# Kernel tuning notes

Hardware: AMD Instinct MI355X
Metric: run time of the kernel (lower is better)

## Reference

```python
import jax, jax.numpy as jnp
import numpy as np

B, S, D, H, L = 2, 2048, 1024, 16, 4
HD = D // H
EPS = 1e-6
ROPE_BASE = 10000.0


def rms_norm(x, w):
    v = jnp.mean(x.astype(jnp.float32) ** 2, axis=-1, keepdims=True)
    return (w * (x.astype(jnp.float32) * jax.lax.rsqrt(v + EPS))).astype(x.dtype)


def rotate_half(x):
    x1, x2 = jnp.split(x, 2, axis=-1)
    return jnp.concatenate([-x2, x1], axis=-1)


def setup_inputs() -> dict:
    key = jax.random.key(0)
    ks = jax.random.split(key, 8)
    x = jax.random.normal(ks[0], (B, S, D), jnp.float32)
    time_deltas = jax.random.uniform(ks[1], (B, S), jnp.float32)
    # causal multiplicative mask [B, S, S]
    attn_mask = jnp.broadcast_to(jnp.tril(jnp.ones((S, S), jnp.float32)), (B, S, S))
    sd = 0.02
    uvqk_w = jax.random.normal(ks[2], (L, D, 4 * D), jnp.float32) * sd
    uvqk_b = jnp.zeros((L, 4 * D), jnp.float32)
    gate_w = jnp.ones((L, D), jnp.float32)
    out_w = jax.random.normal(ks[3], (L, D, D), jnp.float32) * sd
    out_b = jnp.zeros((L, D), jnp.float32)
    in_norm_w = jnp.ones((D,), jnp.float32)
    last_norm_w = jnp.ones((D,), jnp.float32)
    position_ids = jnp.broadcast_to(jnp.arange(S, dtype=jnp.int32), (B, S))
    return {"x": x, "time_deltas": time_deltas, "attn_mask": attn_mask,
            "uvqk_w": uvqk_w, "uvqk_b": uvqk_b, "gate_w": gate_w,
            "out_w": out_w, "out_b": out_b, "in_norm_w": in_norm_w,
            "last_norm_w": last_norm_w, "position_ids": position_ids}


def reference(x, time_deltas, attn_mask, uvqk_w, uvqk_b, gate_w, out_w, out_b,
              in_norm_w, last_norm_w, position_ids):
    # RotaryEmbedding: combined position = pos + 0.1*log(dt+1)
    inv_freq = 1.0 / ROPE_BASE ** (jnp.arange(0, HD, 2, dtype=jnp.float32) / HD)
    pos = position_ids.astype(jnp.float32) + jnp.log(time_deltas + 1.0) * 0.1
    freqs = pos[..., None] * inv_freq                      # [B,S,HD/2]
    emb = jnp.concatenate([freqs, freqs], axis=-1)          # [B,S,HD]
    cos = jnp.cos(emb)[:, :, None, :]                       # [B,S,1,HD]
    sin = jnp.sin(emb)[:, :, None, :]

    scale = 1.0 / np.sqrt(HD).astype(np.float32)
    h = rms_norm(x, in_norm_w)
    for l in range(L):
        residual = h
        uvqk = h @ uvqk_w[l] + uvqk_b[l]                    # [B,S,4D]
        u, v, q, k = jnp.split(uvqk, 4, axis=-1)
        u = jax.nn.silu(u)
        q = q.reshape(B, S, H, HD)
        k = k.reshape(B, S, H, HD)
        v = v.reshape(B, S, H, HD)
        q = q * cos + rotate_half(q) * sin
        k = k * cos + rotate_half(k) * sin
        scores = jnp.einsum('bqhd,bkhd->bhqk', q, k) * scale
        w = jax.nn.silu(scores) * attn_mask[:, None, :, :]  # SiLU attn, masked
        attn = jnp.einsum('bhqk,bkhd->bqhd', w, v).reshape(B, S, D)
        gated = rms_norm(attn, gate_w[l]) * u
        h = residual + gated @ out_w[l] + out_b[l]
    return rms_norm(h, last_norm_w)
```

## Files before the change

kernel.cpp:

```cpp
#include <hip/hip_runtime.h>
#include <hip/hip_bf16.h>
#include <math.h>

#define BB 2
#define SS 2048
#define DD 1024
#define HH 16
#define HD 64
#define LL 4
#define BS (BB * SS)
#define FOURD (4 * DD)

typedef unsigned int u32;
typedef unsigned short ushort_t;
typedef __attribute__((ext_vector_type(8))) short bf16x8;
typedef __attribute__((ext_vector_type(4))) float f32x4;

__device__ __forceinline__ float silu_f(float x) {
    return x / (1.0f + expf(-x));
}
__device__ __forceinline__ float silu_fast(float x) {
    return x / (1.0f + __expf(-x));
}

__device__ __forceinline__ ushort_t f2bf(float x) {
    u32 u = __float_as_uint(x);
    u32 r = (u + 0x7fffu + ((u >> 16) & 1u)) >> 16;
    return (ushort_t)r;
}
__device__ __forceinline__ float bf2f(ushort_t h) {
    return __uint_as_float((u32)h << 16);
}

typedef __attribute__((address_space(3))) u32 lds_u32;
typedef const __attribute__((address_space(1))) u32 glb_u32;
__device__ __forceinline__ void gload16(const void* g, const void* lds) {
    __builtin_amdgcn_global_load_lds((glb_u32*)(uintptr_t)g,
                                     (lds_u32*)(uintptr_t)lds, 16, 0, 0);
}

#define MFMA16(a, b, c) __builtin_amdgcn_mfma_f32_16x16x32_bf16((a), (b), (c), 0, 0, 0)

union U8 { u32 d[4]; bf16x8 v; };

__global__ __launch_bounds__(256) void rope_table_kernel(
    const float* __restrict__ td, const int* __restrict__ pid,
    float* __restrict__ cosT, float* __restrict__ sinT)
{
    int idx = blockIdx.x * blockDim.x + threadIdx.x;
    if (idx >= BS * 32) return;
    int i = idx & 31, bs = idx >> 5;
    float pos = (float)pid[bs] + 0.1f * logf(td[bs] + 1.0f);
    float inv = powf(10000.0f, -(float)(2 * i) / 64.0f);
    float f = pos * inv;
    float c = cosf(f), s = sinf(f);
    cosT[bs * HD + i] = c;  cosT[bs * HD + i + 32] = c;
    sinT[bs * HD + i] = s;  sinT[bs * HD + i + 32] = s;
}

__global__ __launch_bounds__(256) void rmsnorm_kernel(
    const float* __restrict__ in, const float* __restrict__ w,
    const float* __restrict__ mul, int mulStride,
    float* __restrict__ out,
    ushort_t* __restrict__ hi, ushort_t* __restrict__ lo)
{
    __shared__ float red[4];
    int row = blockIdx.x, t = threadIdx.x;
    const float4 v = *(const float4*)&in[(size_t)row * DD + t * 4];
    float ss = v.x * v.x + v.y * v.y + v.z * v.z + v.w * v.w;
    #pragma unroll
    for (int o = 32; o > 0; o >>= 1) ss += __shfl_down(ss, o);
    if ((t & 63) == 0) red[t >> 6] = ss;
    __syncthreads();
    float tot = red[0] + red[1] + red[2] + red[3];
    float r = rsqrtf(tot * (1.0f / (float)DD) + 1e-6f);
    const float4 wv = *(const float4*)&w[t * 4];
    float4 o4;
    o4.x = v.x * r * wv.x;  o4.y = v.y * r * wv.y;
    o4.z = v.z * r * wv.z;  o4.w = v.w * r * wv.w;
    if (mul) {
        const float4 m = *(const float4*)&mul[(size_t)row * mulStride + t * 4];
        o4.x *= m.x; o4.y *= m.y; o4.z *= m.z; o4.w *= m.w;
    }
    const size_t o = (size_t)row * DD + t * 4;
    *(float4*)&out[o] = o4;
    if (hi) {
        ushort4 h4, l4;
        float e;
        h4.x = f2bf(o4.x); e = o4.x - bf2f(h4.x); l4.x = f2bf(e);
        h4.y = f2bf(o4.y); e = o4.y - bf2f(h4.y); l4.y = f2bf(e);
        h4.z = f2bf(o4.z); e = o4.z - bf2f(h4.z); l4.z = f2bf(e);
        h4.w = f2bf(o4.w); e = o4.w - bf2f(h4.w); l4.w = f2bf(e);
        *(ushort4*)&hi[o] = h4;
        *(ushort4*)&lo[o] = l4;
    }
}

__global__ __launch_bounds__(256) void wsplit_kernel(
    const float* __restrict__ W, ushort_t* __restrict__ hi,
    ushort_t* __restrict__ lo, int K, int N)
{
    __shared__ float T[32][33];
    const int n0 = blockIdx.x * 32, k0 = blockIdx.y * 32;
    const int t = threadIdx.x;
    {
        const int r = t >> 3, cg = (t & 7) * 4;
        const float4 v = *(const float4*)&W[(size_t)(k0 + r) * N + n0 + cg];
        T[r][cg] = v.x; T[r][cg + 1] = v.y; T[r][cg + 2] = v.z; T[r][cg + 3] = v.w;
    }
    __syncthreads();
    {
        const int n = t >> 3, kg = (t & 7) * 4;
        ushort4 h4, l4;
        float x, e;
        x = T[kg + 0][n]; h4.x = f2bf(x); e = x - bf2f(h4.x); l4.x = f2bf(e);
        x = T[kg + 1][n]; h4.y = f2bf(x); e = x - bf2f(h4.y); l4.y = f2bf(e);
        x = T[kg + 2][n]; h4.z = f2bf(x); e = x - bf2f(h4.z); l4.z = f2bf(e);
        x = T[kg + 3][n]; h4.w = f2bf(x); e = x - bf2f(h4.w); l4.w = f2bf(e);
        const size_t o = (size_t)(n0 + n) * K + k0 + kg;
        *(ushort4*)&hi[o] = h4;
        *(ushort4*)&lo[o] = l4;
    }
}

#define TBM 128
#define TBN 128
#define TBK 32
__global__ __launch_bounds__(256) void gemm3_kernel(
    const ushort_t* __restrict__ Ah, const ushort_t* __restrict__ Al,
    const ushort_t* __restrict__ Bh, const ushort_t* __restrict__ Bl,
    const float* __restrict__ bias, const float* __restrict__ res,
    float* __restrict__ C, ushort_t* __restrict__ Chi, ushort_t* __restrict__ Clo,
    int M, int N, int K)
{
    __shared__ ushort_t sAh[TBM][TBK];
    __shared__ ushort_t sAl[TBM][TBK];
    __shared__ ushort_t sBh[TBN][TBK];
    __shared__ ushort_t sBl[TBN][TBK];

    const int tid = threadIdx.x;
    const int w = tid >> 6, l = tid & 63;
    const int wr = w >> 1, wc = w & 1;
    const int m0 = blockIdx.y * TBM, n0 = blockIdx.x * TBN;
    const int lr = l & 15, lk = (l >> 4) * 8;

    f32x4 acc[4][4];
    #pragma unroll
    for (int m = 0; m < 4; ++m)
        #pragma unroll
        for (int n = 0; n < 4; ++n)
            acc[m][n] = (f32x4){0.f, 0.f, 0.f, 0.f};

    for (int k0 = 0; k0 < K; k0 += TBK) {
        if (k0) __syncthreads();
        #pragma unroll
        for (int i = 0; i < 2; ++i) {
            const int cb = i * 256 + w * 64;
            const int chunk = cb + l;
            const int row = chunk >> 2;
            const int kc = (chunk & 3) * 8;
            const size_t ga = (size_t)(m0 + row) * K + k0 + kc;
            const size_t gb = (size_t)(n0 + row) * K + k0 + kc;
            gload16(Ah + ga, &sAh[0][0] + (size_t)cb * 8);
            gload16(Al + ga, &sAl[0][0] + (size_t)cb * 8);
            gload16(Bh + gb, &sBh[0][0] + (size_t)cb * 8);
            gload16(Bl + gb, &sBl[0][0] + (size_t)cb * 8);
        }
        __syncthreads();

        bf16x8 ah[4], al[4], bh[4], bl[4];
        #pragma unroll
        for (int m = 0; m < 4; ++m) {
            ah[m] = *(const bf16x8*)&sAh[wr * 64 + m * 16 + lr][lk];
            al[m] = *(const bf16x8*)&sAl[wr * 64 + m * 16 + lr][lk];
        }
        #pragma unroll
        for (int n = 0; n < 4; ++n) {
            bh[n] = *(const bf16x8*)&sBh[wc * 64 + n * 16 + lr][lk];
            bl[n] = *(const bf16x8*)&sBl[wc * 64 + n * 16 + lr][lk];
        }
        #pragma unroll
        for (int m = 0; m < 4; ++m) {
            #pragma unroll
            for (int n = 0; n < 4; ++n) {
                acc[m][n] = MFMA16(ah[m], bh[n], acc[m][n]);
                acc[m][n] = MFMA16(al[m], bh[n], acc[m][n]);
                acc[m][n] = MFMA16(ah[m], bl[n], acc[m][n]);
            }
        }
    }

    #pragma unroll
    for (int m = 0; m < 4; ++m) {
        #pragma unroll
        for (int n = 0; n < 4; ++n) {
            const int col = n0 + wc * 64 + n * 16 + lr;
            #pragma unroll
            for (int r = 0; r < 4; ++r) {
                const int row = m0 + wr * 64 + m * 16 + (l >> 4) * 4 + r;
                const size_t o = (size_t)row * N + col;
                float v = acc[m][n][r] + bias[col];
                if (res) v += res[o];
                C[o] = v;
                if (Chi) {
                    ushort_t hv = f2bf(v);
                    Chi[o] = hv;
                    Clo[o] = f2bf(v - bf2f(hv));
                }
            }
        }
    }
}

__global__ __launch_bounds__(256) void postproc_kernel(
    float* __restrict__ uvqk,
    const float* __restrict__ cosT, const float* __restrict__ sinT,
    ushort_t* __restrict__ q_hi, ushort_t* __restrict__ q_lo,
    ushort_t* __restrict__ k_hi, ushort_t* __restrict__ k_lo)
{
    const int bs = blockIdx.x, t = threadIdx.x;
    const int b = bs >> 11, s = bs & (SS - 1);
    float* base = uvqk + (size_t)bs * FOURD;

    float4 u = *(float4*)&base[t * 4];
    u.x = silu_f(u.x); u.y = silu_f(u.y); u.z = silu_f(u.z); u.w = silu_f(u.w);
    *(float4*)&base[t * 4] = u;

    const int hh = t >> 4, p = (t & 15) * 2;
    const float c0 = cosT[bs * HD + p], c1 = cosT[bs * HD + p + 1];
    const float s0 = sinT[bs * HD + p], s1 = sinT[bs * HD + p + 1];
    const size_t hrow = ((size_t)(b * HH + hh) * SS + s) * HD;
    #pragma unroll
    for (int sect = 2; sect <= 3; ++sect) {
        const float* qp = base + sect * DD + hh * HD;
        const float a0 = qp[p], a1 = qp[p + 1];
        const float b0 = qp[p + 32], b1 = qp[p + 33];
        float o0 = a0 * c0 - b0 * s0;
        float o1 = a1 * c1 - b1 * s1;
        float o2 = b0 * c0 + a0 * s0;
        float o3 = b1 * c1 + a1 * s1;
        ushort_t* dh = (sect == 2) ? q_hi : k_hi;
        ushort_t* dl = (sect == 2) ? q_lo : k_lo;
        ushort_t hv;
        hv = f2bf(o0); dh[hrow + p]      = hv; dl[hrow + p]      = f2bf(o0 - bf2f(hv));
        hv = f2bf(o1); dh[hrow + p + 1]  = hv; dl[hrow + p + 1]  = f2bf(o1 - bf2f(hv));
        hv = f2bf(o2); dh[hrow + p + 32] = hv; dl[hrow + p + 32] = f2bf(o2 - bf2f(hv));
        hv = f2bf(o3); dh[hrow + p + 33] = hv; dl[hrow + p + 33] = f2bf(o3 - bf2f(hv));
    }
}

__global__ __launch_bounds__(256) void vtrans_kernel(
    const float* __restrict__ uvqk,
    ushort_t* __restrict__ vT_hi, ushort_t* __restrict__ vT_lo)
{
    __shared__ float T[64][65];
    const int sb = blockIdx.x, h = blockIdx.y, b = blockIdx.z;
    const int t = threadIdx.x;
    const int s0 = sb * 64;
    #pragma unroll
    for (int it = 0; it < 4; ++it) {
        const int idx = it * 256 + t;
        const int row = idx >> 4, c4 = (idx & 15) * 4;
        const float4 v = *(const float4*)&uvqk[
            (size_t)(b * SS + s0 + row) * FOURD + DD + h * HD + c4];
        T[row][c4] = v.x; T[row][c4 + 1] = v.y;
        T[row][c4 + 2] = v.z; T[row][c4 + 3] = v.w;
    }
    __syncthreads();
    const int d = t >> 2, sc = (t & 3) * 16;
    u32 hw[8], lw[8];
    #pragma unroll
    for (int j = 0; j < 8; ++j) {
        const float x0 = T[sc + 2 * j][d];
        const float x1 = T[sc + 2 * j + 1][d];
        const ushort_t h0 = f2bf(x0), h1 = f2bf(x1);
        hw[j] = (u32)h0 | ((u32)h1 << 16);
        lw[j] = (u32)f2bf(x0 - bf2f(h0)) | ((u32)f2bf(x1 - bf2f(h1)) << 16);
    }
    const size_t o = ((size_t)(b * HH + h) * HD + d) * SS + s0 + sc;
    *(uint4*)&vT_hi[o] = make_uint4(hw[0], hw[1], hw[2], hw[3]);
    *(uint4*)&vT_hi[o + 8] = make_uint4(hw[4], hw[5], hw[6], hw[7]);
    *(uint4*)&vT_lo[o] = make_uint4(lw[0], lw[1], lw[2], lw[3]);
    *(uint4*)&vT_lo[o + 8] = make_uint4(lw[4], lw[5], lw[6], lw[7]);
}

__global__ __launch_bounds__(256) void attn_kernel(
    const ushort_t* __restrict__ q_hi, const ushort_t* __restrict__ q_lo,
    const ushort_t* __restrict__ k_hi, const ushort_t* __restrict__ k_lo,
    const ushort_t* __restrict__ vT_hi, const ushort_t* __restrict__ vT_lo,
    float* __restrict__ attnOut)
{
    __shared__ ushort_t sKh[2][64 * 64];
    __shared__ ushort_t sKl[2][64 * 64];
    __shared__ ushort_t sVh[2][64 * 64];
    __shared__ ushort_t sVl[2][64 * 64];

    const int qt = (SS / 128 - 1) - blockIdx.x;
    const int h = blockIdx.y, b = blockIdx.z;
    const int tid = threadIdx.x;
    const int w = tid >> 6, l = tid & 63;
    const int lr = l & 15, g = l >> 4;

    const size_t headQ = ((size_t)(b * HH + h) * SS) * HD;
    const size_t headV = ((size_t)(b * HH + h) * HD) * SS;

    bf16x8 qh[2][2], ql[2][2];
    {
        const int qrow0 = qt * 128 + w * 32;
        #pragma unroll
        for (int qf = 0; qf < 2; ++qf)
            #pragma unroll
            for (int ds_ = 0; ds_ < 2; ++ds_) {
                const size_t off = headQ + (size_t)(qrow0 + qf * 16 + lr) * HD
                                   + ds_ * 32 + g * 8;
                qh[qf][ds_] = *(const bf16x8*)&q_hi[off];
                ql[qf][ds_] = *(const bf16x8*)&q_lo[off];
            }
    }

    f32x4 acc[2][4];
    #pragma unroll
    for (int qf = 0; qf < 2; ++qf)
        #pragma unroll
        for (int df = 0; df < 4; ++df)
            acc[qf][df] = (f32x4){0.f, 0.f, 0.f, 0.f};

    const int nkt = 2 * qt + 2;

#define STAGE_TILE(pb, kt_)                                                    \
    {                                                                          \
        const ushort_t* kbh = k_hi + headQ + (size_t)(kt_) * 64 * HD;          \
        const ushort_t* kbl = k_lo + headQ + (size_t)(kt_) * 64 * HD;          \
        const ushort_t* vbh = vT_hi + headV + (kt_) * 64;                      \
        const ushort_t* vbl = vT_lo + headV + (kt_) * 64;                      \
        _Pragma("unroll")                                                      \
        for (int rep = 0; rep < 2; ++rep) {                                    \
            const int cb = rep * 256 + w * 64;                                 \
            const int chunk = cb + l;                                          \
            const int row = chunk >> 3, dblk = chunk & 7;                      \
            const int sblk = dblk ^ (row & 7);                                 \
            gload16(kbh + (size_t)row * HD + sblk * 8, &sKh[pb][0] + (size_t)cb * 8); \
            gload16(kbl + (size_t)row * HD + sblk * 8, &sKl[pb][0] + (size_t)cb * 8); \
            gload16(vbh + (size_t)row * SS + sblk * 8, &sVh[pb][0] + (size_t)cb * 8); \
            gload16(vbl + (size_t)row * SS + sblk * 8, &sVl[pb][0] + (size_t)cb * 8); \
        }                                                                      \
    }

    STAGE_TILE(0, 0)
    __syncthreads();

    for (int kt = 0; kt < nkt; ++kt) {
        const int pb = kt & 1;
        if (kt + 1 < nkt) STAGE_TILE(pb ^ 1, kt + 1)

        f32x4 sc[4][2];
        #pragma unroll
        for (int f = 0; f < 4; ++f)
            #pragma unroll
            for (int qf = 0; qf < 2; ++qf)
                sc[f][qf] = (f32x4){0.f, 0.f, 0.f, 0.f};

        #pragma unroll
        for (int ds_ = 0; ds_ < 2; ++ds_) {
            bf16x8 kh[4], kl[4];
            #pragma unroll
            for (int f = 0; f < 4; ++f) {
                const int addr = (16 * f + lr) * 64 + (((4 * ds_ + g) ^ (lr & 7)) * 8);
                kh[f] = *(const bf16x8*)&sKh[pb][addr];
                kl[f] = *(const bf16x8*)&sKl[pb][addr];
            }
            #pragma unroll
            for (int f = 0; f < 4; ++f)
                #pragma unroll
                for (int qf = 0; qf < 2; ++qf) {
                    sc[f][qf] = MFMA16(kh[f], qh[qf][ds_], sc[f][qf]);
                    sc[f][qf] = MFMA16(kl[f], qh[qf][ds_], sc[f][qf]);
                    sc[f][qf] = MFMA16(kh[f], ql[qf][ds_], sc[f][qf]);
                }
        }

        u32 pkh[4][2][2], pkl[4][2][2];
        #pragma unroll
        for (int f = 0; f < 4; ++f) {
            #pragma unroll
            for (int qf = 0; qf < 2; ++qf) {
                const int qrow = qt * 128 + w * 32 + qf * 16 + lr;
                float pv[4];
                #pragma unroll
                for (int r = 0; r < 4; ++r) {
                    const int key = kt * 64 + 16 * f + 4 * g + r;
                    const float x = sc[f][qf][r] * 0.125f;
                    pv[r] = (key <= qrow) ? silu_fast(x) : 0.0f;
                }
                #pragma unroll
                for (int t2 = 0; t2 < 2; ++t2) {
                    const ushort_t h0 = f2bf(pv[2 * t2]);
                    const ushort_t h1 = f2bf(pv[2 * t2 + 1]);
                    pkh[f][qf][t2] = (u32)h0 | ((u32)h1 << 16);
                    const float l0 = pv[2 * t2] - bf2f(h0);
                    const float l1 = pv[2 * t2 + 1] - bf2f(h1);
                    pkl[f][qf][t2] = (u32)f2bf(l0) | ((u32)f2bf(l1) << 16);
                }
            }
        }

        #pragma unroll
        for (int s2 = 0; s2 < 2; ++s2) {
            U8 ah[2], al[2];
            #pragma unroll
            for (int qf = 0; qf < 2; ++qf) {
                #pragma unroll
                for (int d = 0; d < 4; ++d) {
                    const int srcLane = lr + 16 * (2 * (g & 1) + (d >> 1));
                    const int t2 = d & 1;
                    int x0 = __shfl((int)pkh[2 * s2][qf][t2], srcLane, 64);
                    int x1 = __shfl((int)pkh[2 * s2 + 1][qf][t2], srcLane, 64);
                    ah[qf].d[d] = (g & 2) ? x1 : x0;
                    x0 = __shfl((int)pkl[2 * s2][qf][t2], srcLane, 64);
                    x1 = __shfl((int)pkl[2 * s2 + 1][qf][t2], srcLane, 64);
                    al[qf].d[d] = (g & 2) ? x1 : x0;
                }
            }
            #pragma unroll
            for (int df = 0; df < 4; ++df) {
                const int vaddr = (16 * df + lr) * 64 + (((4 * s2 + g) ^ (lr & 7)) * 8);
                const bf16x8 vh = *(const bf16x8*)&sVh[pb][vaddr];
                const bf16x8 vl = *(const bf16x8*)&sVl[pb][vaddr];
                #pragma unroll
                for (int qf = 0; qf < 2; ++qf) {
                    acc[qf][df] = MFMA16(ah[qf].v, vh, acc[qf][df]);
                    acc[qf][df] = MFMA16(al[qf].v, vh, acc[qf][df]);
                    acc[qf][df] = MFMA16(ah[qf].v, vl, acc[qf][df]);
                }
            }
        }

        __syncthreads();
    }

    #pragma unroll
    for (int qf = 0; qf < 2; ++qf) {
        #pragma unroll
        for (int df = 0; df < 4; ++df) {
            #pragma unroll
            for (int r = 0; r < 4; ++r) {
                const int row = qt * 128 + w * 32 + qf * 16 + 4 * g + r;
                attnOut[(size_t)(b * SS + row) * DD + h * HD + 16 * df + lr]
                    = acc[qf][df][r];
            }
        }
    }
#undef STAGE_TILE
}

extern "C" void kernel_launch(void* const* d_in, const int* in_sizes, int n_in,
                              void* d_out, int out_size, void* d_ws, size_t ws_size,
                              hipStream_t stream) {
    const float* x           = (const float*)d_in[0];
    const float* td          = (const float*)d_in[1];
    const float* uvqk_w      = (const float*)d_in[3];
    const float* uvqk_b      = (const float*)d_in[4];
    const float* gate_w      = (const float*)d_in[5];
    const float* out_w       = (const float*)d_in[6];
    const float* out_b       = (const float*)d_in[7];
    const float* in_norm_w   = (const float*)d_in[8];
    const float* last_norm_w = (const float*)d_in[9];
    const int*   pid         = (const int*)d_in[10];
    float* out = (float*)d_out;
    char*  ws  = (char*)d_ws;

    const size_t QKV = (size_t)BB * HH * SS * HD;

    float* cosT = (float*)ws;                          ws += (size_t)BS * HD * 4;
    float* sinT = (float*)ws;                          ws += (size_t)BS * HD * 4;
    float* h    = (float*)ws;                          ws += (size_t)BS * DD * 4;
    float* uvqk = (float*)ws;                          ws += (size_t)BS * FOURD * 4;
    float* attn = (float*)ws;                          ws += (size_t)BS * DD * 4;
    ushort_t* h_hi  = (ushort_t*)ws;                   ws += (size_t)BS * DD * 2;
    ushort_t* h_lo  = (ushort_t*)ws;                   ws += (size_t)BS * DD * 2;
    ushort_t* g_hi  = (ushort_t*)ws;                   ws += (size_t)BS * DD * 2;
    ushort_t* g_lo  = (ushort_t*)ws;                   ws += (size_t)BS * DD * 2;
    ushort_t* uWt_hi = (ushort_t*)ws;                  ws += (size_t)FOURD * DD * 2;
    ushort_t* uWt_lo = (ushort_t*)ws;                  ws += (size_t)FOURD * DD * 2;
    ushort_t* oWt_hi = (ushort_t*)ws;                  ws += (size_t)DD * DD * 2;
    ushort_t* oWt_lo = (ushort_t*)ws;                  ws += (size_t)DD * DD * 2;
    ushort_t* q_hi  = (ushort_t*)ws;                   ws += QKV * 2;
    ushort_t* q_lo  = (ushort_t*)ws;                   ws += QKV * 2;
    ushort_t* k_hi  = (ushort_t*)ws;                   ws += QKV * 2;
    ushort_t* k_lo  = (ushort_t*)ws;                   ws += QKV * 2;
    ushort_t* vT_hi = (ushort_t*)ws;                   ws += QKV * 2;
    ushort_t* vT_lo = (ushort_t*)ws;                   ws += QKV * 2;
    (void)ws_size;

    rope_table_kernel<<<(BS * 32 + 255) / 256, 256, 0, stream>>>(td, pid, cosT, sinT);
    rmsnorm_kernel<<<BS, 256, 0, stream>>>(x, in_norm_w, nullptr, 0, h, h_hi, h_lo);

    for (int l = 0; l < LL; ++l) {
        wsplit_kernel<<<dim3(FOURD / 32, DD / 32), 256, 0, stream>>>(
            uvqk_w + (size_t)l * DD * FOURD, uWt_hi, uWt_lo, DD, FOURD);
        gemm3_kernel<<<dim3(FOURD / TBN, BS / TBM), 256, 0, stream>>>(
            h_hi, h_lo, uWt_hi, uWt_lo, uvqk_b + (size_t)l * FOURD,
            nullptr, uvqk, nullptr, nullptr, BS, FOURD, DD);
        postproc_kernel<<<BS, 256, 0, stream>>>(
            uvqk, cosT, sinT, q_hi, q_lo, k_hi, k_lo);
        vtrans_kernel<<<dim3(SS / 64, HH, BB), 256, 0, stream>>>(
            uvqk, vT_hi, vT_lo);
        attn_kernel<<<dim3(SS / 128, HH, BB), 256, 0, stream>>>(
            q_hi, q_lo, k_hi, k_lo, vT_hi, vT_lo, attn);
        rmsnorm_kernel<<<BS, 256, 0, stream>>>(
            attn, gate_w + (size_t)l * DD, uvqk, FOURD, attn, g_hi, g_lo);
        wsplit_kernel<<<dim3(DD / 32, DD / 32), 256, 0, stream>>>(
            out_w + (size_t)l * DD * DD, oWt_hi, oWt_lo, DD, DD);
        gemm3_kernel<<<dim3(DD / TBN, BS / TBM), 256, 0, stream>>>(
            g_hi, g_lo, oWt_hi, oWt_lo, out_b + (size_t)l * DD,
            h, h, h_hi, h_lo, BS, DD, DD);
    }

    rmsnorm_kernel<<<BS, 256, 0, stream>>>(h, last_norm_w, nullptr, 0, out, nullptr, nullptr);
}
```

Baseline: 1.667 ms.

## Skip fully-masked warp tiles, truncate bf16 splits, balance batch tile order

In the attention kernel, each warp now skips score and PV compute for key tiles lying entirely above its causal diagonal. The hi/lo bf16 split of P switches from round-to-nearest to truncation, which is cheaper but leaves the low part carrying the truncation error. SiLU uses a hardware reciprocal instead of a divide. Batch 1 walks query tiles in the opposite order to batch 0 to balance causal load across blocks. The RoPE kernel packs bf16 pairs into 32-bit stores. Truncation and the approximate reciprocal slightly change numerics.

After: 1.490 ms. -10.6%, faster.

```diff
diff --git a/kernel.cpp b/kernel.cpp
--- a/kernel.cpp
+++ b/kernel.cpp
@@ -20,7 +20,7 @@
     return x / (1.0f + expf(-x));
 }
 __device__ __forceinline__ float silu_fast(float x) {
-    return x / (1.0f + __expf(-x));
+    return x * __builtin_amdgcn_rcpf(1.0f + __expf(-x));
 }
 
 __device__ __forceinline__ ushort_t f2bf(float x) {
@@ -241,11 +241,14 @@
         float o3 = b1 * c1 + a1 * s1;
         ushort_t* dh = (sect == 2) ? q_hi : k_hi;
         ushort_t* dl = (sect == 2) ? q_lo : k_lo;
-        ushort_t hv;
-        hv = f2bf(o0); dh[hrow + p]      = hv; dl[hrow + p]      = f2bf(o0 - bf2f(hv));
-        hv = f2bf(o1); dh[hrow + p + 1]  = hv; dl[hrow + p + 1]  = f2bf(o1 - bf2f(hv));
-        hv = f2bf(o2); dh[hrow + p + 32] = hv; dl[hrow + p + 32] = f2bf(o2 - bf2f(hv));
-        hv = f2bf(o3); dh[hrow + p + 33] = hv; dl[hrow + p + 33] = f2bf(o3 - bf2f(hv));
+        const ushort_t h0 = f2bf(o0), h1 = f2bf(o1);
+        const ushort_t h2 = f2bf(o2), h3 = f2bf(o3);
+        *(u32*)&dh[hrow + p]      = (u32)h0 | ((u32)h1 << 16);
+        *(u32*)&dh[hrow + p + 32] = (u32)h2 | ((u32)h3 << 16);
+        *(u32*)&dl[hrow + p]      = (u32)f2bf(o0 - bf2f(h0))
+                                  | ((u32)f2bf(o1 - bf2f(h1)) << 16);
+        *(u32*)&dl[hrow + p + 32] = (u32)f2bf(o2 - bf2f(h2))
+                                  | ((u32)f2bf(o3 - bf2f(h3)) << 16);
     }
 }
 
@@ -295,8 +298,8 @@
     __shared__ ushort_t sVh[2][64 * 64];
     __shared__ ushort_t sVl[2][64 * 64];
 
-    const int qt = (SS / 128 - 1) - blockIdx.x;
     const int h = blockIdx.y, b = blockIdx.z;
+    const int qt = b ? blockIdx.x : (SS / 128 - 1) - blockIdx.x;
     const int tid = threadIdx.x;
     const int w = tid >> 6, l = tid & 63;
     const int lr = l & 15, g = l >> 4;
@@ -353,6 +356,8 @@
         const int pb = kt & 1;
         if (kt + 1 < nkt) STAGE_TILE(pb ^ 1, kt + 1)
 
+        if (kt * 64 <= qt * 128 + w * 32 + 31) {
+
         f32x4 sc[4][2];
         #pragma unroll
         for (int f = 0; f < 4; ++f)
@@ -394,12 +399,14 @@
                 }
                 #pragma unroll
                 for (int t2 = 0; t2 < 2; ++t2) {
-                    const ushort_t h0 = f2bf(pv[2 * t2]);
-                    const ushort_t h1 = f2bf(pv[2 * t2 + 1]);
-                    pkh[f][qf][t2] = (u32)h0 | ((u32)h1 << 16);
-                    const float l0 = pv[2 * t2] - bf2f(h0);
-                    const float l1 = pv[2 * t2 + 1] - bf2f(h1);
-                    pkl[f][qf][t2] = (u32)f2bf(l0) | ((u32)f2bf(l1) << 16);
+                    const u32 u0 = __float_as_uint(pv[2 * t2]);
+                    const u32 u1 = __float_as_uint(pv[2 * t2 + 1]);
+                    const u32 h0 = u0 >> 16, h1 = u1 >> 16;
+                    pkh[f][qf][t2] = h0 | (h1 << 16);
+                    const float l0 = pv[2 * t2]     - __uint_as_float(h0 << 16);
+                    const float l1 = pv[2 * t2 + 1] - __uint_as_float(h1 << 16);
+                    pkl[f][qf][t2] = (__float_as_uint(l0) >> 16)
+                                   | ((__float_as_uint(l1) >> 16) << 16);
                 }
             }
         }
@@ -433,6 +440,8 @@
                     acc[qf][df] = MFMA16(ah[qf].v, vl, acc[qf][df]);
                 }
             }
+        }
+
         }
 
         __syncthreads();
```
